# Performance work log

Measured on AMD Instinct MI355X. Metric: run time of the kernel, lower is better.

## Reference

```python
import jax, jax.numpy as jnp
import numpy as np

EPS = 1e-05


def setup_inputs() -> dict:
    key = jax.random.key(0)
    k1, _ = jax.random.split(key)
    x = jax.random.normal(k1, (4, 8192, 1024), dtype=jnp.float32)
    weight = jnp.ones((1024,), dtype=jnp.float32)
    return {"x": x, "weight": weight}


def reference(x, weight):
    # GMRNorm, elementwise=True path. The original computes, per channel c,
    # mean[b,t,c] = sum_{s<=t} x[b,s,c] / (t+1) via a [T,T] triangular matmul,
    # with the (0,0) entry zeroed so mean at t=0 is 0. This is exactly a
    # cumulative sum divided by the prefix count, computed here in O(B*T*C).
    x = x.astype(jnp.float32)
    B, T, C = x.shape
    counts = jnp.arange(1, T + 1, dtype=jnp.float32)[:, None]  # [T,1]
    mean = jnp.cumsum(x, axis=1) / counts                      # [B,T,C]
    mean = mean.at[:, 0, :].set(0.0)                           # causal_matrix[0,0] = 0
    xc = x - mean
    norm_x = jnp.mean(xc * xc, axis=-1, keepdims=True)         # per-timestep variance over C
    x_normed = xc * jax.lax.rsqrt(norm_x + EPS)
    return weight * x_normed
```

## Files before the change

### kernel.cpp

```cpp
#include <hip/hip_runtime.h>

#define T_    8192
#define C_    1024
#define TCH   8
#define NCH   (T_ / TCH)
#define SBS   8
#define NSB   (NCH / SBS)
#define BATCH 4

__global__ __launch_bounds__(256) void k_sumscan(const float* __restrict__ x,
                                                 float* __restrict__ S,
                                                 float* __restrict__ S2) {
    const int sb = blockIdx.x;
    const int b  = blockIdx.y;
    const int c  = threadIdx.x * 4;
    const float* xp = x + ((size_t)(b * T_ + sb * SBS * TCH) * C_ + c);
    float* Sp = S + ((size_t)(b * NCH + sb * SBS) * C_ + c);
    float4 run = make_float4(0.f, 0.f, 0.f, 0.f);
#pragma unroll
    for (int j = 0; j < SBS; ++j) {
        *(float4*)(Sp + (size_t)j * C_) = run;
        float4 v[TCH];
#pragma unroll
        for (int i = 0; i < TCH; ++i)
            v[i] = *(const float4*)(xp + (size_t)(j * TCH + i) * C_);
#pragma unroll
        for (int i = 0; i < TCH; ++i) {
            run.x += v[i].x; run.y += v[i].y; run.z += v[i].z; run.w += v[i].w;
        }
    }
    *(float4*)(S2 + ((size_t)(b * NSB + sb) * C_ + c)) = run;
}

__global__ __launch_bounds__(256) void k_scan_b(float* __restrict__ S2) {
    const int idx = blockIdx.x * 256 + threadIdx.x;
    const int c = idx & (C_ - 1);
    const int b = idx >> 10;
    float* p = S2 + ((size_t)b * NSB * C_ + c);
    float run = 0.f;
#pragma unroll 8
    for (int j = 0; j < NSB; ++j) {
        float v = p[(size_t)j * C_];
        p[(size_t)j * C_] = run;
        run += v;
    }
}

__global__ __launch_bounds__(256, 3) void k_norm(const float* __restrict__ x,
                                                 const float* __restrict__ S,
                                                 const float* __restrict__ S2,
                                                 const float* __restrict__ w,
                                                 float* __restrict__ out) {
    const int wave = threadIdx.x >> 6;
    const int lane = threadIdx.x & 63;
    const int ch   = blockIdx.x * 4 + wave;
    const int b    = blockIdx.y;
    const int cb   = lane * 4;

    float4 run[4], wt[4];
    const float* Pp  = S  + (size_t)(b * NCH + ch) * C_;
    const float* P2p = S2 + (size_t)(b * NSB + (ch / SBS)) * C_;
#pragma unroll
    for (int q = 0; q < 4; ++q) {
        float4 a  = *(const float4*)(Pp  + q * 256 + cb);
        float4 bb = *(const float4*)(P2p + q * 256 + cb);
        run[q] = make_float4(a.x + bb.x, a.y + bb.y, a.z + bb.z, a.w + bb.w);
        wt[q]  = *(const float4*)(w + q * 256 + cb);
    }

    const int t0 = ch * TCH;
    const float* xp = x   + (size_t)(b * T_ + t0) * C_;
    float*       op = out + (size_t)(b * T_ + t0) * C_;
    const float invC = 1.0f / (float)C_;

#pragma unroll
    for (int h = 0; h < TCH / BATCH; ++h) {
        float4 xc[BATCH][4];
        float  sq[BATCH];

#pragma unroll
        for (int i = 0; i < BATCH; ++i) {
            const int tt = t0 + h * BATCH + i;
            const float m = (tt == 0) ? 0.0f
                                      : __builtin_amdgcn_rcpf((float)(tt + 1));
            float s = 0.f;
#pragma unroll
            for (int q = 0; q < 4; ++q) {
                float4 v = *(const float4*)(xp + (size_t)(h * BATCH + i) * C_
                                               + q * 256 + cb);
                run[q].x += v.x; float a0 = v.x - run[q].x * m; s += a0 * a0;
                run[q].y += v.y; float a1 = v.y - run[q].y * m; s += a1 * a1;
                run[q].z += v.z; float a2 = v.z - run[q].z * m; s += a2 * a2;
                run[q].w += v.w; float a3 = v.w - run[q].w * m; s += a3 * a3;
                xc[i][q] = make_float4(a0, a1, a2, a3);
            }
            sq[i] = s;
        }

#pragma unroll
        for (int off = 32; off; off >>= 1) {
#pragma unroll
            for (int i = 0; i < BATCH; ++i)
                sq[i] += __shfl_xor(sq[i], off, 64);
        }

        float scale[BATCH];
#pragma unroll
        for (int i = 0; i < BATCH; ++i)
            scale[i] = __builtin_amdgcn_rsqf(sq[i] * invC + 1e-5f);

#pragma unroll
        for (int i = 0; i < BATCH; ++i) {
#pragma unroll
            for (int q = 0; q < 4; ++q) {
                float4 o;
                o.x = wt[q].x * xc[i][q].x * scale[i];
                o.y = wt[q].y * xc[i][q].y * scale[i];
                o.z = wt[q].z * xc[i][q].z * scale[i];
                o.w = wt[q].w * xc[i][q].w * scale[i];
                *(float4*)(op + (size_t)(h * BATCH + i) * C_ + q * 256 + cb) = o;
            }
        }
    }
}

extern "C" void kernel_launch(void* const* d_in, const int* in_sizes, int n_in,
                              void* d_out, int out_size, void* d_ws, size_t ws_size,
                              hipStream_t stream) {
    const float* x = (const float*)d_in[0];
    const float* w = (const float*)d_in[1];
    float* out = (float*)d_out;

    const int B = in_sizes[0] / (T_ * C_);

    float* S  = (float*)d_ws;
    float* S2 = S + (size_t)B * NCH * C_;

    dim3 g1(NSB, B);
    k_sumscan<<<g1, 256, 0, stream>>>(x, S, S2);

    const int nb = B * C_;
    k_scan_b<<<nb / 256, 256, 0, stream>>>(S2);

    dim3 g2(NCH / 4, B);
    k_norm<<<g2, 256, 0, stream>>>(x, S, S2, w, out);
}
```

Measured before the change: 267.1 us.

## Enlarge time chunks, parallelize block scan with wave shuffles, use nontemporal stores

Result: faster. 261.0 us (-2.3%).

```diff
diff --git a/kernel.cpp b/kernel.cpp
--- a/kernel.cpp
+++ b/kernel.cpp
@@ -2,11 +2,13 @@
 
 #define T_    8192
 #define C_    1024
-#define TCH   8
+#define TCH   16
 #define NCH   (T_ / TCH)
-#define SBS   8
+#define SBS   4
 #define NSB   (NCH / SBS)
 #define BATCH 4
+
+typedef float v4f __attribute__((ext_vector_type(4)));
 
 __global__ __launch_bounds__(256) void k_sumscan(const float* __restrict__ x,
                                                  float* __restrict__ S,
@@ -20,37 +22,60 @@
 #pragma unroll
     for (int j = 0; j < SBS; ++j) {
         *(float4*)(Sp + (size_t)j * C_) = run;
-        float4 v[TCH];
 #pragma unroll
-        for (int i = 0; i < TCH; ++i)
-            v[i] = *(const float4*)(xp + (size_t)(j * TCH + i) * C_);
+        for (int hh = 0; hh < 2; ++hh) {
+            float4 v[8];
 #pragma unroll
-        for (int i = 0; i < TCH; ++i) {
-            run.x += v[i].x; run.y += v[i].y; run.z += v[i].z; run.w += v[i].w;
+            for (int i = 0; i < 8; ++i)
+                v[i] = *(const float4*)(xp + (size_t)(j * TCH + hh * 8 + i) * C_);
+#pragma unroll
+            for (int i = 0; i < 8; ++i) {
+                run.x += v[i].x; run.y += v[i].y;
+                run.z += v[i].z; run.w += v[i].w;
+            }
         }
     }
     *(float4*)(S2 + ((size_t)(b * NSB + sb) * C_ + c)) = run;
 }
 
-__global__ __launch_bounds__(256) void k_scan_b(float* __restrict__ S2) {
-    const int idx = blockIdx.x * 256 + threadIdx.x;
-    const int c = idx & (C_ - 1);
-    const int b = idx >> 10;
-    float* p = S2 + ((size_t)b * NSB * C_ + c);
-    float run = 0.f;
-#pragma unroll 8
-    for (int j = 0; j < NSB; ++j) {
-        float v = p[(size_t)j * C_];
-        p[(size_t)j * C_] = run;
-        run += v;
+__global__ __launch_bounds__(256) void k_scan2(float* __restrict__ S2, int B) {
+    const int wid  = blockIdx.x * 4 + (threadIdx.x >> 6);
+    const int lane = threadIdx.x & 63;
+    if (wid >= B * C_) return;
+    const int b = wid >> 10;
+    const int c = wid & (C_ - 1);
+    float* base = S2 + ((size_t)b * NSB * C_ + c);
+
+    float v0 = base[(size_t)lane * C_];
+    float v1 = base[(size_t)(64 + lane) * C_];
+
+#pragma unroll
+    for (int off = 1; off < 64; off <<= 1) {
+        float t = __shfl_up(v0, off, 64);
+        if (lane >= off) v0 += t;
     }
+    const float total0 = __shfl(v0, 63, 64);
+
+#pragma unroll
+    for (int off = 1; off < 64; off <<= 1) {
+        float t = __shfl_up(v1, off, 64);
+        if (lane >= off) v1 += t;
+    }
+    v1 += total0;
+
+    float e0 = __shfl_up(v0, 1, 64);
+    if (lane == 0) e0 = 0.f;
+    float e1 = __shfl_up(v1, 1, 64);
+    if (lane == 0) e1 = total0;
+    base[(size_t)lane * C_]        = e0;
+    base[(size_t)(64 + lane) * C_] = e1;
 }
 
-__global__ __launch_bounds__(256, 3) void k_norm(const float* __restrict__ x,
-                                                 const float* __restrict__ S,
-                                                 const float* __restrict__ S2,
-                                                 const float* __restrict__ w,
-                                                 float* __restrict__ out) {
+__global__ __launch_bounds__(256) void k_norm(const float* __restrict__ x,
+                                              const float* __restrict__ S,
+                                              const float* __restrict__ S2,
+                                              const float* __restrict__ w,
+                                              float* __restrict__ out) {
     const int wave = threadIdx.x >> 6;
     const int lane = threadIdx.x & 63;
     const int ch   = blockIdx.x * 4 + wave;
@@ -113,12 +138,13 @@
         for (int i = 0; i < BATCH; ++i) {
 #pragma unroll
             for (int q = 0; q < 4; ++q) {
-                float4 o;
+                v4f o;
                 o.x = wt[q].x * xc[i][q].x * scale[i];
                 o.y = wt[q].y * xc[i][q].y * scale[i];
                 o.z = wt[q].z * xc[i][q].z * scale[i];
                 o.w = wt[q].w * xc[i][q].w * scale[i];
-                *(float4*)(op + (size_t)(h * BATCH + i) * C_ + q * 256 + cb) = o;
+                __builtin_nontemporal_store(o,
+                    (v4f*)(op + (size_t)(h * BATCH + i) * C_ + q * 256 + cb));
             }
         }
     }
@@ -139,8 +165,8 @@
     dim3 g1(NSB, B);
     k_sumscan<<<g1, 256, 0, stream>>>(x, S, S2);
 
-    const int nb = B * C_;
-    k_scan_b<<<nb / 256, 256, 0, stream>>>(S2);
+    const int nwaves = B * C_;
+    k_scan2<<<nwaves / 4, 256, 0, stream>>>(S2, B);
 
     dim3 g2(NCH / 4, B);
     k_norm<<<g2, 256, 0, stream>>>(x, S, S2, w, out);
```

## Fuse three-kernel scan and norm into single decoupled-lookback kernel

Applied to the files above, without the earlier changes.

Result: slower. 479.6 us (+79.6%).

```diff
diff --git a/kernel.cpp b/kernel.cpp
--- a/kernel.cpp
+++ b/kernel.cpp
@@ -2,74 +2,91 @@
 
 #define T_    8192
 #define C_    1024
-#define TCH   8
-#define NCH   (T_ / TCH)
-#define SBS   8
-#define NSB   (NCH / SBS)
+#define TCH   16
+#define CPB   4
+#define ROWS  (CPB * TCH)
+#define NSB   (T_ / ROWS)
 #define BATCH 4
 
-__global__ __launch_bounds__(256) void k_sumscan(const float* __restrict__ x,
-                                                 float* __restrict__ S,
-                                                 float* __restrict__ S2) {
-    const int sb = blockIdx.x;
-    const int b  = blockIdx.y;
-    const int c  = threadIdx.x * 4;
-    const float* xp = x + ((size_t)(b * T_ + sb * SBS * TCH) * C_ + c);
-    float* Sp = S + ((size_t)(b * NCH + sb * SBS) * C_ + c);
+typedef float v4f __attribute__((ext_vector_type(4)));
+
+__global__ __launch_bounds__(256, 2) void k_all(const float* __restrict__ x,
+                                                float* __restrict__ agg,
+                                                float* __restrict__ inc,
+                                                int*   __restrict__ flags,
+                                                const float* __restrict__ w,
+                                                float* __restrict__ out) {
+    const int sb  = blockIdx.x;
+    const int b   = blockIdx.y;
+    const int tid = threadIdx.x;
+
+    __shared__ float chunkpre[CPB][C_];
+    __shared__ float pre2[C_];
+
+    const int c4 = tid * 4;
+    const float* xp = x + ((size_t)(b * T_ + sb * ROWS)) * C_ + c4;
     float4 run = make_float4(0.f, 0.f, 0.f, 0.f);
 #pragma unroll
-    for (int j = 0; j < SBS; ++j) {
-        *(float4*)(Sp + (size_t)j * C_) = run;
-        float4 v[TCH];
-#pragma unroll
-        for (int i = 0; i < TCH; ++i)
-            v[i] = *(const float4*)(xp + (size_t)(j * TCH + i) * C_);
+    for (int j = 0; j < CPB; ++j) {
+        *(float4*)&chunkpre[j][c4] = run;
 #pragma unroll
         for (int i = 0; i < TCH; ++i) {
-            run.x += v[i].x; run.y += v[i].y; run.z += v[i].z; run.w += v[i].w;
+            float4 v = *(const float4*)(xp + (size_t)(j * TCH + i) * C_);
+            run.x += v.x; run.y += v.y; run.z += v.z; run.w += v.w;
         }
     }
-    *(float4*)(S2 + ((size_t)(b * NSB + sb) * C_ + c)) = run;
-}
 
-__global__ __launch_bounds__(256) void k_scan_b(float* __restrict__ S2) {
-    const int idx = blockIdx.x * 256 + threadIdx.x;
-    const int c = idx & (C_ - 1);
-    const int b = idx >> 10;
-    float* p = S2 + ((size_t)b * NSB * C_ + c);
-    float run = 0.f;
-#pragma unroll 8
-    for (int j = 0; j < NSB; ++j) {
-        float v = p[(size_t)j * C_];
-        p[(size_t)j * C_] = run;
-        run += v;
+    const size_t tile = (size_t)b * NSB + sb;
+    float4 excl = make_float4(0.f, 0.f, 0.f, 0.f);
+
+    if (sb > 0) {
+        *(float4*)(agg + tile * C_ + c4) = run;
+        __syncthreads();
+        if (tid == 0)
+            __hip_atomic_store(&flags[tile], 1, __ATOMIC_RELEASE,
+                               __HIP_MEMORY_SCOPE_AGENT);
+        int t = sb - 1;
+        while (true) {
+            const size_t pt = (size_t)b * NSB + t;
+            int f;
+            do {
+                f = __hip_atomic_load(&flags[pt], __ATOMIC_ACQUIRE,
+                                      __HIP_MEMORY_SCOPE_AGENT);
+            } while (f == 0);
+            const float* src = (f == 2 ? inc : agg) + pt * C_ + c4;
+            float4 v = *(const float4*)src;
+            excl.x += v.x; excl.y += v.y; excl.z += v.z; excl.w += v.w;
+            if (f == 2 || t == 0) break;
+            --t;
+        }
+        float4 iv = make_float4(excl.x + run.x, excl.y + run.y,
+                                excl.z + run.z, excl.w + run.w);
+        *(float4*)(inc + tile * C_ + c4) = iv;
+    } else {
+        *(float4*)(inc + tile * C_ + c4) = run;
     }
-}
+    *(float4*)&pre2[c4] = excl;
+    __syncthreads();
+    if (tid == 0)
+        __hip_atomic_store(&flags[tile], 2, __ATOMIC_RELEASE,
+                           __HIP_MEMORY_SCOPE_AGENT);
 
-__global__ __launch_bounds__(256, 3) void k_norm(const float* __restrict__ x,
-                                                 const float* __restrict__ S,
-                                                 const float* __restrict__ S2,
-                                                 const float* __restrict__ w,
-                                                 float* __restrict__ out) {
-    const int wave = threadIdx.x >> 6;
-    const int lane = threadIdx.x & 63;
-    const int ch   = blockIdx.x * 4 + wave;
-    const int b    = blockIdx.y;
+    const int wave = tid >> 6;
+    const int lane = tid & 63;
+    const int ch   = sb * CPB + wave;
     const int cb   = lane * 4;
 
-    float4 run[4], wt[4];
-    const float* Pp  = S  + (size_t)(b * NCH + ch) * C_;
-    const float* P2p = S2 + (size_t)(b * NSB + (ch / SBS)) * C_;
+    float4 racc[4], wt[4];
 #pragma unroll
     for (int q = 0; q < 4; ++q) {
-        float4 a  = *(const float4*)(Pp  + q * 256 + cb);
-        float4 bb = *(const float4*)(P2p + q * 256 + cb);
-        run[q] = make_float4(a.x + bb.x, a.y + bb.y, a.z + bb.z, a.w + bb.w);
-        wt[q]  = *(const float4*)(w + q * 256 + cb);
+        float4 p2 = *(const float4*)&pre2[q * 256 + cb];
+        float4 cp = *(const float4*)&chunkpre[wave][q * 256 + cb];
+        racc[q] = make_float4(p2.x + cp.x, p2.y + cp.y, p2.z + cp.z, p2.w + cp.w);
+        wt[q]   = *(const float4*)(w + q * 256 + cb);
     }
 
     const int t0 = ch * TCH;
-    const float* xp = x   + (size_t)(b * T_ + t0) * C_;
+    const float* xq = x   + (size_t)(b * T_ + t0) * C_;
     float*       op = out + (size_t)(b * T_ + t0) * C_;
     const float invC = 1.0f / (float)C_;
 
@@ -86,12 +103,12 @@
             float s = 0.f;
 #pragma unroll
             for (int q = 0; q < 4; ++q) {
-                float4 v = *(const float4*)(xp + (size_t)(h * BATCH + i) * C_
+                float4 v = *(const float4*)(xq + (size_t)(h * BATCH + i) * C_
                                                + q * 256 + cb);
-                run[q].x += v.x; float a0 = v.x - run[q].x * m; s += a0 * a0;
-                run[q].y += v.y; float a1 = v.y - run[q].y * m; s += a1 * a1;
-                run[q].z += v.z; float a2 = v.z - run[q].z * m; s += a2 * a2;
-                run[q].w += v.w; float a3 = v.w - run[q].w * m; s += a3 * a3;
+                racc[q].x += v.x; float a0 = v.x - racc[q].x * m; s += a0 * a0;
+                racc[q].y += v.y; float a1 = v.y - racc[q].y * m; s += a1 * a1;
+                racc[q].z += v.z; float a2 = v.z - racc[q].z * m; s += a2 * a2;
+                racc[q].w += v.w; float a3 = v.w - racc[q].w * m; s += a3 * a3;
                 xc[i][q] = make_float4(a0, a1, a2, a3);
             }
             sq[i] = s;
@@ -113,12 +130,13 @@
         for (int i = 0; i < BATCH; ++i) {
 #pragma unroll
             for (int q = 0; q < 4; ++q) {
-                float4 o;
+                v4f o;
                 o.x = wt[q].x * xc[i][q].x * scale[i];
                 o.y = wt[q].y * xc[i][q].y * scale[i];
                 o.z = wt[q].z * xc[i][q].z * scale[i];
                 o.w = wt[q].w * xc[i][q].w * scale[i];
-                *(float4*)(op + (size_t)(h * BATCH + i) * C_ + q * 256 + cb) = o;
+                __builtin_nontemporal_store(o,
+                    (v4f*)(op + (size_t)(h * BATCH + i) * C_ + q * 256 + cb));
             }
         }
     }
@@ -133,15 +151,12 @@
 
     const int B = in_sizes[0] / (T_ * C_);
 
-    float* S  = (float*)d_ws;
-    float* S2 = S + (size_t)B * NCH * C_;
+    float* agg   = (float*)d_ws;
+    float* inc   = agg + (size_t)B * NSB * C_;
+    int*   flags = (int*)(inc + (size_t)B * NSB * C_);
 
-    dim3 g1(NSB, B);
-    k_sumscan<<<g1, 256, 0, stream>>>(x, S, S2);
+    hipMemsetAsync(flags, 0, (size_t)B * NSB * sizeof(int), stream);
 
-    const int nb = B * C_;
-    k_scan_b<<<nb / 256, 256, 0, stream>>>(S2);
-
-    dim3 g2(NCH / 4, B);
-    k_norm<<<g2, 256, 0, stream>>>(x, S, S2, w, out);
+    dim3 g(NSB, B);
+    k_all<<<g, 256, 0, stream>>>(x, agg, inc, flags, w, out);
 }
```
